# Optimization experiments

Measured on AMD Instinct MI355X. Metric: run time of the kernel, lower is better.

## Reference

```python
import jax, jax.numpy as jnp
import numpy as np

N_EMBD = 1024
N_HEAD = 16
HEAD_SIZE = 64

def setup_inputs() -> dict:
    key = jax.random.key(0)
    ks = jax.random.split(key, 6)
    B, T = 4, 2048
    x = jax.random.normal(ks[0], (B, T, N_EMBD), dtype=jnp.float32)
    s = 1.0 / np.sqrt(N_EMBD)
    Wq = jax.random.normal(ks[1], (N_HEAD, N_EMBD, HEAD_SIZE), dtype=jnp.float32) * s
    Wk = jax.random.normal(ks[2], (N_HEAD, N_EMBD, HEAD_SIZE), dtype=jnp.float32) * s
    Wv = jax.random.normal(ks[3], (N_HEAD, N_EMBD, HEAD_SIZE), dtype=jnp.float32) * s
    Wp = jax.random.normal(ks[4], (N_EMBD, N_EMBD), dtype=jnp.float32) * s
    bp = jax.random.normal(ks[5], (N_EMBD,), dtype=jnp.float32) * 0.01
    return {"x": x, "Wq": Wq, "Wk": Wk, "Wv": Wv, "Wp": Wp, "bp": bp}

def reference(x, Wq, Wk, Wv, Wp, bp):
    B, T, C = x.shape
    # per-head projections, all heads at once: [B,H,T,hs]
    q = jnp.einsum('btc,hcd->bhtd', x, Wq)
    k = jnp.einsum('btc,hcd->bhtd', x, Wk)
    v = jnp.einsum('btc,hcd->bhtd', x, Wv)
    # NOTE: original scales by C**-0.5 with C = n_embd (not head_size)
    scale = C ** (-0.5)
    wei = jnp.einsum('bhtd,bhsd->bhts', q, k) * scale  # [B,H,T,T]
    causal = jnp.tril(jnp.ones((T, T), dtype=bool))
    wei = jnp.where(causal, wei, -jnp.inf)
    wei = jax.nn.softmax(wei, axis=-1)
    out = jnp.einsum('bhts,bhsd->bhtd', wei, v)  # [B,H,T,hs]
    out = out.transpose(0, 2, 1, 3).reshape(B, T, -1)  # concat heads -> [B,T,C]
    return out @ Wp + bp
```

## Files before the change

kernel.cpp:

```cpp
#include <hip/hip_runtime.h>
#include <stdint.h>
#include <math.h>

typedef short s16x8 __attribute__((ext_vector_type(8)));
typedef float f32x4 __attribute__((ext_vector_type(4)));
typedef float f32x16 __attribute__((ext_vector_type(16)));

__device__ __forceinline__ unsigned short f2bf(float f) {
    union { float f; uint32_t u; } x; x.f = f;
    uint32_t r = x.u + 0x7FFFu + ((x.u >> 16) & 1u);
    return (unsigned short)(r >> 16);
}

__device__ __forceinline__ uint32_t cvtpk_bf16(float lo, float hi) {
    uint32_t r;
    asm("v_cvt_pk_bf16_f32 %0, %1, %2" : "=v"(r) : "v"(lo), "v"(hi));
    return r;
}

#define GLD_LDS16(gp, lp) __builtin_amdgcn_global_load_lds( \
    (const __attribute__((address_space(1))) uint32_t*)(gp), \
    (__attribute__((address_space(3))) uint32_t*)(lp), 16, 0, 0)

#define MFMA16x16x32(a, b, c) __builtin_amdgcn_mfma_f32_16x16x32_bf16((a), (b), (c), 0, 0, 0)
#define MFMA32x32x16(a, b, c) __builtin_amdgcn_mfma_f32_32x32x16_bf16((a), (b), (c), 0, 0, 0)

__device__ __forceinline__ void plswap(uint32_t a, uint32_t b, int lh, uint32_t& x, uint32_t& y) {
#if __has_builtin(__builtin_amdgcn_permlane32_swap)
    auto r = __builtin_amdgcn_permlane32_swap(a, b, false, false);
    x = (uint32_t)r[0]; y = (uint32_t)r[1];
#else
    uint32_t as = (uint32_t)__shfl_xor((int)a, 32, 64);
    uint32_t bs = (uint32_t)__shfl_xor((int)b, 32, 64);
    x = lh ? bs : a;
    y = lh ? b : as;
#endif
}

__global__ void cvt_x_kernel(const float* __restrict__ x, unsigned short* __restrict__ xb, int n) {
    int i = (blockIdx.x * blockDim.x + threadIdx.x) * 4;
    if (i >= n) return;
    float4 v = *(const float4*)(x + i);
    unsigned short o0 = f2bf(v.x), o1 = f2bf(v.y), o2 = f2bf(v.z), o3 = f2bf(v.w);
    uint64_t packed = (uint64_t)o0 | ((uint64_t)o1 << 16) | ((uint64_t)o2 << 32) | ((uint64_t)o3 << 48);
    *(uint64_t*)(xb + i) = packed;
}

__global__ void cvt_w_kernel(const float* __restrict__ Wq, const float* __restrict__ Wk,
                             const float* __restrict__ Wv, const float* __restrict__ Wp,
                             unsigned short* __restrict__ WtQKV, unsigned short* __restrict__ WtP) {
    int id = (blockIdx.x * blockDim.x + threadIdx.x) * 4;
    int which = id >> 20, rem = id & 1048575;
    const float* src = (which == 0) ? Wq : (which == 1) ? Wk : (which == 2) ? Wv : Wp;
    float4 v = *(const float4*)(src + rem);
    unsigned short* dst;
    if (which < 3) {
        int h = rem >> 16, c = (rem >> 6) & 1023, d = rem & 63;
        dst = WtQKV + (size_t)(which * 1024 + h * 64 + d) * 1024 + c;
    } else {
        int c = rem >> 10, n = rem & 1023;
        dst = WtP + (size_t)n * 1024 + c;
    }
    dst[0] = f2bf(v.x); dst[1024] = f2bf(v.y); dst[2048] = f2bf(v.z); dst[3072] = f2bf(v.w);
}

__global__ __launch_bounds__(512, 4) void gemm_qkv_kernel(
    const unsigned short* __restrict__ A, const unsigned short* __restrict__ Bt,
    unsigned short* __restrict__ qkv2, unsigned short* __restrict__ vT)
{
    constexpr int K = 1024, NT = 32;
    __shared__ __align__(16) unsigned short LA[3][128 * 32];
    __shared__ __align__(16) unsigned short LB[3][256 * 32];

    const int t = threadIdx.x, w = t >> 6, l = t & 63, lr = l & 15, lg = l >> 4;
    const int wm2 = w >> 2, wn4 = w & 3;

    int bid = blockIdx.x;
    int swz = (bid & 7) * 96 + (bid >> 3);
    const int bm = (swz & 63) << 7, bn = (swz >> 6) << 8;

    const unsigned short* Ab = A + (size_t)bm * K;
    const unsigned short* Bb = Bt + (size_t)bn * K;

    int sArow, sAce, sBrow[2], sBce[2];
    {
        int u = t >> 4, x = (t & 15) ^ (u & 15);
        sArow = 4 * u + (x >> 2); sAce = (x & 3) << 3;
        #pragma unroll
        for (int i2 = 0; i2 < 2; ++i2) {
            int i = t + i2 * 512;
            int ub = i >> 4, xb2 = (i & 15) ^ (ub & 15);
            sBrow[i2] = 4 * ub + (xb2 >> 2); sBce[i2] = (xb2 & 3) << 3;
        }
    }

    int aoff[4], boff[4];
    #pragma unroll
    for (int m = 0; m < 4; ++m) {
        int u = 16 * wm2 + 4 * m + (lr >> 2);
        aoff[m] = u * 256 + (((lg + 4 * (lr & 3)) ^ (u & 15)) << 4);
    }
    #pragma unroll
    for (int n = 0; n < 4; ++n) {
        int u = 16 * wn4 + 4 * n + (lr >> 2);
        boff[n] = u * 256 + (((lg + 4 * (lr & 3)) ^ (u & 15)) << 4);
    }

    f32x4 acc[4][4] = {};

    GLD_LDS16(Ab + (size_t)sArow * K + 0 + sAce, &LA[0][t * 8]);
    #pragma unroll
    for (int i2 = 0; i2 < 2; ++i2)
        GLD_LDS16(Bb + (size_t)sBrow[i2] * K + 0 + sBce[i2], &LB[0][(t + i2 * 512) * 8]);
    GLD_LDS16(Ab + (size_t)sArow * K + 32 + sAce, &LA[1][t * 8]);
    #pragma unroll
    for (int i2 = 0; i2 < 2; ++i2)
        GLD_LDS16(Bb + (size_t)sBrow[i2] * K + 32 + sBce[i2], &LB[1][(t + i2 * 512) * 8]);
    asm volatile("s_waitcnt vmcnt(3)" ::: "memory");
    __builtin_amdgcn_sched_barrier(0);
    __builtin_amdgcn_s_barrier();

    int cur = 0;
    for (int j = 0; j < NT; ++j) {
        const int dst = (cur >= 1) ? cur - 1 : cur + 2;
        const bool st = (j + 2 < NT);
        const int k2 = (j + 2) << 5;
        s16x8 af[4], bfr[4];
        #pragma unroll
        for (int m = 0; m < 4; ++m)
            af[m] = *(const s16x8*)((const char*)LA[cur] + aoff[m]);
        #pragma unroll
        for (int n = 0; n < 4; ++n)
            bfr[n] = *(const s16x8*)((const char*)LB[cur] + boff[n]);
        if (st) {
            GLD_LDS16(Ab + (size_t)sArow * K + k2 + sAce, &LA[dst][t * 8]);
            #pragma unroll
            for (int i2 = 0; i2 < 2; ++i2)
                GLD_LDS16(Bb + (size_t)sBrow[i2] * K + k2 + sBce[i2], &LB[dst][(t + i2 * 512) * 8]);
        }
        __builtin_amdgcn_s_barrier();
        asm volatile("s_waitcnt lgkmcnt(0)" ::: "memory");
        __builtin_amdgcn_sched_barrier(0);
        __builtin_amdgcn_s_setprio(1);
        #pragma unroll
        for (int m = 0; m < 4; ++m)
            #pragma unroll
            for (int n = 0; n < 4; ++n)
                acc[m][n] = MFMA16x16x32(af[m], bfr[n], acc[m][n]);
        __builtin_amdgcn_s_setprio(0);
        if (j + 1 < NT) {
            if (st) { asm volatile("s_waitcnt vmcnt(3)" ::: "memory"); }
            else    { asm volatile("s_waitcnt vmcnt(0)" ::: "memory"); }
            __builtin_amdgcn_sched_barrier(0);
        }
        __builtin_amdgcn_s_barrier();
        cur = (cur == 2) ? 0 : cur + 1;
    }

    const bool isV = (bn >= 2048);
    const float sc = (bn < 1024) ? (0.03125f * 1.44269504088896341f) : 1.0f;
    #pragma unroll
    for (int mi = 0; mi < 4; ++mi)
        #pragma unroll
        for (int ni = 0; ni < 4; ++ni) {
            int col = bn + wn4 * 64 + ni * 16 + lr;
            int row0 = bm + wm2 * 64 + mi * 16 + lg * 4;
            if (!isV) {
                #pragma unroll
                for (int r = 0; r < 4; ++r)
                    qkv2[(size_t)(row0 + r) * 2048 + col] = f2bf(acc[mi][ni][r] * sc);
            } else {
                int h = (col >> 6) & 15, d = col & 63;
                size_t vb = ((size_t)((row0 >> 11) * 16 + h) * 64 + d) * 2048 + (row0 & 2047);
                uint32_t u0 = (uint32_t)f2bf(acc[mi][ni][0]) | ((uint32_t)f2bf(acc[mi][ni][1]) << 16);
                uint32_t u1 = (uint32_t)f2bf(acc[mi][ni][2]) | ((uint32_t)f2bf(acc[mi][ni][3]) << 16);
                *(uint32_t*)&vT[vb]     = u0;
                *(uint32_t*)&vT[vb + 2] = u1;
            }
        }
}

__global__ __launch_bounds__(256) void gemm_proj_kernel(
    const unsigned short* __restrict__ A, const unsigned short* __restrict__ Bt,
    float* __restrict__ C, const float* __restrict__ bias, int M, int N, int K)
{
    constexpr int BK = 64;
    __shared__ __align__(16) unsigned short As[128 * BK];
    __shared__ __align__(16) unsigned short Bs[128 * BK];
    const int t = threadIdx.x, w = t >> 6, l = t & 63, lr = l & 15, lg = l >> 4;
    const int wm = (w >> 1) << 6, wn = (w & 1) << 6;
    const int bm = blockIdx.x << 7, bn = blockIdx.y << 7;
    const unsigned short* Ab = A + (size_t)bm * K;
    const unsigned short* Bb = Bt + (size_t)bn * K;
    f32x4 acc[4][4] = {};
    for (int k0 = 0; k0 < K; k0 += BK) {
        __syncthreads();
        #pragma unroll
        for (int i = 0; i < 4; ++i) {
            int c = i * 256 + t;
            GLD_LDS16(Ab + (size_t)(c >> 3) * K + k0 + ((c & 7) << 3), As + c * 8);
        }
        #pragma unroll
        for (int i = 0; i < 4; ++i) {
            int c = i * 256 + t;
            GLD_LDS16(Bb + (size_t)(c >> 3) * K + k0 + ((c & 7) << 3), Bs + c * 8);
        }
        __syncthreads();
        #pragma unroll
        for (int ks = 0; ks < 2; ++ks) {
            s16x8 af[4], bfr[4];
            #pragma unroll
            for (int mi = 0; mi < 4; ++mi)
                af[mi] = *(const s16x8*)&As[(wm + mi * 16 + lr) * BK + ks * 32 + lg * 8];
            #pragma unroll
            for (int ni = 0; ni < 4; ++ni)
                bfr[ni] = *(const s16x8*)&Bs[(wn + ni * 16 + lr) * BK + ks * 32 + lg * 8];
            #pragma unroll
            for (int mi = 0; mi < 4; ++mi)
                #pragma unroll
                for (int ni = 0; ni < 4; ++ni)
                    acc[mi][ni] = MFMA16x16x32(af[mi], bfr[ni], acc[mi][ni]);
        }
    }
    #pragma unroll
    for (int mi = 0; mi < 4; ++mi)
        #pragma unroll
        for (int ni = 0; ni < 4; ++ni) {
            int col = bn + wn + ni * 16 + lr;
            float bv = bias[col];
            #pragma unroll
            for (int r = 0; r < 4; ++r) {
                int row = bm + wm + mi * 16 + lg * 4 + r;
                C[(size_t)row * N + col] = acc[mi][ni][r] + bv;
            }
        }
}

__device__ __forceinline__ void proc32(
    const unsigned short* __restrict__ Ksb, const unsigned short* __restrict__ Vtb,
    const s16x8* qf, f32x16* o, float& m_r, float& l_r,
    int qms, bool domask, int lq, int lh)
{
    const int ub = lq >> 1;
    const int vb8 = (lq & 1) << 3;
    f32x16 S[2] = {};
    __builtin_amdgcn_s_setprio(1);
    #pragma unroll
    for (int sblk = 0; sblk < 2; ++sblk)
        #pragma unroll
        for (int kd = 0; kd < 4; ++kd) {
            s16x8 kf = *(const s16x8*)((const char*)Ksb + (sblk * 16 + ub) * 256
                                       + ((((2 * kd + lh) + vb8) ^ ub) << 4));
            S[sblk] = MFMA32x32x16(kf, qf[kd], S[sblk]);
        }
    __builtin_amdgcn_s_setprio(0);
    if (domask) {
        #pragma unroll
        for (int sblk = 0; sblk < 2; ++sblk)
            #pragma unroll
            for (int r = 0; r < 16; ++r) {
                int s_loc = sblk * 32 + (r & 3) + 8 * (r >> 2) + 4 * lh;
                S[sblk][r] = (s_loc <= qms) ? S[sblk][r] : -1e30f;
            }
    }
    float zm = S[0][0];
    #pragma unroll
    for (int r = 1; r < 15; r += 2) zm = fmaxf(fmaxf(zm, S[0][r]), S[0][r + 1]);
    zm = fmaxf(zm, S[0][15]);
    #pragma unroll
    for (int r = 0; r < 16; r += 2) zm = fmaxf(fmaxf(zm, S[1][r]), S[1][r + 1]);
    zm = fmaxf(zm, __shfl_xor(zm, 32, 64));
    const bool defer = (__all(zm <= m_r + 8.0f) != 0);
    if (!defer) {
        float mn = fmaxf(m_r, zm);
        float alpha = exp2f(m_r - mn);
        m_r = mn;
        l_r *= alpha;
        o[0] *= alpha;
        o[1] *= alpha;
    }
    float rs = 0.0f;
    uint32_t pk[2][8];
    #pragma unroll
    for (int sblk = 0; sblk < 2; ++sblk) {
        #pragma unroll
        for (int r = 0; r < 16; ++r) {
            float pv = exp2f(S[sblk][r] - m_r);
            S[sblk][r] = pv;
            rs += pv;
        }
        #pragma unroll
        for (int hh = 0; hh < 8; ++hh)
            pk[sblk][hh] = cvtpk_bf16(S[sblk][2 * hh], S[sblk][2 * hh + 1]);
    }
    rs += __shfl_xor(rs, 32, 64);
    l_r += rs;
    s16x8 pf[4];
    #pragma unroll
    for (int ks2 = 0; ks2 < 4; ++ks2) {
        int sb = ks2 >> 1, Bh = 4 * (ks2 & 1);
        uint32_t w0, w1, w2, w3;
        plswap(pk[sb][Bh + 0], pk[sb][Bh + 2], lh, w0, w2);
        plswap(pk[sb][Bh + 1], pk[sb][Bh + 3], lh, w1, w3);
        union { uint32_t u[4]; s16x8 v; } pu;
        pu.u[0] = w0; pu.u[1] = w1; pu.u[2] = w2; pu.u[3] = w3;
        pf[ks2] = pu.v;
    }
    __builtin_amdgcn_s_setprio(1);
    #pragma unroll
    for (int dblk = 0; dblk < 2; ++dblk)
        #pragma unroll
        for (int ks2 = 0; ks2 < 4; ++ks2) {
            s16x8 vf = *(const s16x8*)((const char*)Vtb + (dblk * 16 + ub) * 256
                                       + ((((2 * ks2 + lh) + vb8) ^ ub) << 4));
            o[dblk] = MFMA32x32x16(vf, pf[ks2], o[dblk]);
        }
    __builtin_amdgcn_s_setprio(0);
}

__global__ __launch_bounds__(512, 4) void attn_kernel(
    const unsigned short* __restrict__ qkv2, const unsigned short* __restrict__ vT,
    unsigned short* __restrict__ attnO, int T)
{
    __shared__ __align__(16) unsigned short Ks[2][64 * 64];
    __shared__ __align__(16) unsigned short Vt[2][64 * 64];

    const int blk = blockIdx.x;
    const int p = blk & 7, h = (blk >> 3) & 15, b = blk >> 7;
    const int q0A = p * 128, q0B = (15 - p) * 128;
    const int nkv = 32 - 2 * p;

    const int t = threadIdx.x, w = t >> 6, l = t & 63, lq = l & 31, lh = l >> 5;
    const int c0 = ((w >> 2) ? q0B : q0A) + 32 * (w & 3);
    const int lastT = (c0 + 31) >> 6;

    const unsigned short* qbase = qkv2 + (size_t)b * T * 2048;
    const unsigned short* kbase = qbase + 1024 + h * 64;
    const unsigned short* vtb   = vT + (size_t)(b * 16 + h) * 64 * 2048;

    s16x8 qf[4];
    #pragma unroll
    for (int kd = 0; kd < 4; ++kd)
        qf[kd] = *(const s16x8*)(qbase + (size_t)(c0 + lq) * 2048 + h * 64 + kd * 16 + lh * 8);

    f32x16 o[2] = {};
    float m_r = -1e30f, l_r = 0.0f;

    const int su = t >> 4, sx = (t & 15) ^ (su & 15);
    const int srow = 2 * su + (sx >> 3), schunk = (sx & 7) << 3;
    auto STAGE = [&](int buf, int s0) {
        GLD_LDS16(kbase + (size_t)(s0 + srow) * 2048 + schunk, &Ks[buf][t * 8]);
        GLD_LDS16(vtb + (size_t)srow * 2048 + s0 + schunk, &Vt[buf][t * 8]);
    };

    STAGE(0, 0);
    __syncthreads();

    for (int kt = 0; kt < nkv; ++kt) {
        const int cur = kt & 1, nxt = cur ^ 1;
        if (kt + 1 < nkv) STAGE(nxt, (kt + 1) * 64);
        if (kt <= lastT)
            proc32(Ks[cur], Vt[cur], qf, o, m_r, l_r, c0 + lq - kt * 64, kt == lastT, lq, lh);
        __syncthreads();
    }

    {
        float inv = 1.0f / l_r;
        #pragma unroll
        for (int dblk = 0; dblk < 2; ++dblk)
            #pragma unroll
            for (int r = 0; r < 16; r += 2) {
                int d = dblk * 32 + (r & 3) + 8 * (r >> 2) + 4 * lh;
                uint32_t ua = cvtpk_bf16(o[dblk][r] * inv, o[dblk][r + 1] * inv);
                *(uint32_t*)&attnO[(size_t)(b * T + c0 + lq) * 1024 + h * 64 + d] = ua;
            }
    }
}

extern "C" void kernel_launch(void* const* d_in, const int* in_sizes, int n_in,
                              void* d_out, int out_size, void* d_ws, size_t ws_size,
                              hipStream_t stream) {
    const float* x  = (const float*)d_in[0];
    const float* Wq = (const float*)d_in[1];
    const float* Wk = (const float*)d_in[2];
    const float* Wv = (const float*)d_in[3];
    const float* Wp = (const float*)d_in[4];
    const float* bp = (const float*)d_in[5];
    float* out = (float*)d_out;

    const int T = 2048, C = 1024;
    const int BT = in_sizes[0] / C;
    const int B  = BT / T;

    char* ws = (char*)d_ws;
    unsigned short* xb    = (unsigned short*)(ws);
    unsigned short* WtQKV = (unsigned short*)(ws + 16777216);
    unsigned short* WtP   = (unsigned short*)(ws + 23068672);
    unsigned short* qkv2  = (unsigned short*)(ws + 25165824);
    unsigned short* vT    = (unsigned short*)(ws + 58720256);
    unsigned short* attn  = (unsigned short*)(ws + 75497472);
    (void)ws_size; (void)n_in; (void)out_size;

    cvt_x_kernel<<<(BT * C / 4 + 255) / 256, 256, 0, stream>>>(x, xb, BT * C);
    cvt_w_kernel<<<4096, 256, 0, stream>>>(Wq, Wk, Wv, Wp, WtQKV, WtP);

    gemm_qkv_kernel<<<768, 512, 0, stream>>>(xb, WtQKV, qkv2, vT);

    attn_kernel<<<B * 16 * 8, 512, 0, stream>>>(qkv2, vT, attn, T);

    gemm_proj_kernel<<<dim3(BT / 128, 1024 / 128), 256, 0, stream>>>(
        attn, WtP, out, bp, BT, 1024, C);
}
```

Measured before the change: 198.4 us.

## Split attention blocks per query tile and compute row sums via MFMA

The attention kernel now launches one 256-thread block per 128-row query tile instead of pairing two tiles (early plus late) in a 512-thread block. Blocks are ordered heaviest-first, with batch/head interleaved across the grid. The softmax denominator is accumulated with an extra MFMA of a bf16 ones vector against the probability fragments, replacing the scalar sum and cross-lane shuffle. This trades the paired load balance for finer, longest-first scheduling and moves the row-sum off the VALU. The sum now uses bf16-rounded probabilities and costs four more MFMAs per tile.

```diff
diff --git a/kernel.cpp b/kernel.cpp
--- a/kernel.cpp
+++ b/kernel.cpp
@@ -238,7 +238,7 @@
 
 __device__ __forceinline__ void proc32(
     const unsigned short* __restrict__ Ksb, const unsigned short* __restrict__ Vtb,
-    const s16x8* qf, f32x16* o, float& m_r, float& l_r,
+    const s16x8* qf, f32x16* o, float& m_r, f32x16& l_acc, s16x8 onesf,
     int qms, bool domask, int lq, int lh)
 {
     const int ub = lq >> 1;
@@ -275,26 +275,20 @@
         float mn = fmaxf(m_r, zm);
         float alpha = exp2f(m_r - mn);
         m_r = mn;
-        l_r *= alpha;
+        l_acc[0] *= alpha;
         o[0] *= alpha;
         o[1] *= alpha;
     }
-    float rs = 0.0f;
     uint32_t pk[2][8];
     #pragma unroll
     for (int sblk = 0; sblk < 2; ++sblk) {
         #pragma unroll
-        for (int r = 0; r < 16; ++r) {
-            float pv = exp2f(S[sblk][r] - m_r);
-            S[sblk][r] = pv;
-            rs += pv;
-        }
+        for (int r = 0; r < 16; ++r)
+            S[sblk][r] = exp2f(S[sblk][r] - m_r);
         #pragma unroll
         for (int hh = 0; hh < 8; ++hh)
             pk[sblk][hh] = cvtpk_bf16(S[sblk][2 * hh], S[sblk][2 * hh + 1]);
     }
-    rs += __shfl_xor(rs, 32, 64);
-    l_r += rs;
     s16x8 pf[4];
     #pragma unroll
     for (int ks2 = 0; ks2 < 4; ++ks2) {
@@ -315,23 +309,28 @@
                                        + ((((2 * ks2 + lh) + vb8) ^ ub) << 4));
             o[dblk] = MFMA32x32x16(vf, pf[ks2], o[dblk]);
         }
+    #pragma unroll
+    for (int ks2 = 0; ks2 < 4; ++ks2)
+        l_acc = MFMA32x32x16(onesf, pf[ks2], l_acc);
     __builtin_amdgcn_s_setprio(0);
 }
 
-__global__ __launch_bounds__(512, 4) void attn_kernel(
+__global__ __launch_bounds__(256, 4) void attn_kernel(
     const unsigned short* __restrict__ qkv2, const unsigned short* __restrict__ vT,
     unsigned short* __restrict__ attnO, int T)
 {
     __shared__ __align__(16) unsigned short Ks[2][64 * 64];
     __shared__ __align__(16) unsigned short Vt[2][64 * 64];
 
-    const int blk = blockIdx.x;
-    const int p = blk & 7, h = (blk >> 3) & 15, b = blk >> 7;
-    const int q0A = p * 128, q0B = (15 - p) * 128;
-    const int nkv = 32 - 2 * p;
+    const int i = blockIdx.x;
+    const int g = i & 7, j = i >> 3;
+    const int tq = 15 - (j >> 3);
+    const int bh = ((j & 7) << 3) | g;
+    const int b = bh >> 4, h = bh & 15;
+    const int nkv = 2 * tq + 2;
 
     const int t = threadIdx.x, w = t >> 6, l = t & 63, lq = l & 31, lh = l >> 5;
-    const int c0 = ((w >> 2) ? q0B : q0A) + 32 * (w & 3);
+    const int c0 = tq * 128 + 32 * w;
     const int lastT = (c0 + 31) >> 6;
 
     const unsigned short* qbase = qkv2 + (size_t)b * T * 2048;
@@ -343,14 +342,30 @@
     for (int kd = 0; kd < 4; ++kd)
         qf[kd] = *(const s16x8*)(qbase + (size_t)(c0 + lq) * 2048 + h * 64 + kd * 16 + lh * 8);
 
-    f32x16 o[2] = {};
-    float m_r = -1e30f, l_r = 0.0f;
-
-    const int su = t >> 4, sx = (t & 15) ^ (su & 15);
-    const int srow = 2 * su + (sx >> 3), schunk = (sx & 7) << 3;
+    f32x16 o[2] = {}, l_acc = {};
+    float m_r = -1e30f;
+    s16x8 onesf;
+    {
+        union { uint32_t u[4]; s16x8 v; } ou;
+        #pragma unroll
+        for (int k2 = 0; k2 < 4; ++k2) ou.u[k2] = 0x3F803F80u;
+        onesf = ou.v;
+    }
+
+    int srow[2], sch[2];
+    #pragma unroll
+    for (int i2 = 0; i2 < 2; ++i2) {
+        int c = t + i2 * 256;
+        int su = c >> 4, sx = (c & 15) ^ (su & 15);
+        srow[i2] = 2 * su + (sx >> 3); sch[i2] = (sx & 7) << 3;
+    }
     auto STAGE = [&](int buf, int s0) {
-        GLD_LDS16(kbase + (size_t)(s0 + srow) * 2048 + schunk, &Ks[buf][t * 8]);
-        GLD_LDS16(vtb + (size_t)srow * 2048 + s0 + schunk, &Vt[buf][t * 8]);
+        #pragma unroll
+        for (int i2 = 0; i2 < 2; ++i2) {
+            int c = t + i2 * 256;
+            GLD_LDS16(kbase + (size_t)(s0 + srow[i2]) * 2048 + sch[i2], &Ks[buf][c * 8]);
+            GLD_LDS16(vtb + (size_t)srow[i2] * 2048 + s0 + sch[i2], &Vt[buf][c * 8]);
+        }
     };
 
     STAGE(0, 0);
@@ -360,12 +375,13 @@
         const int cur = kt & 1, nxt = cur ^ 1;
         if (kt + 1 < nkv) STAGE(nxt, (kt + 1) * 64);
         if (kt <= lastT)
-            proc32(Ks[cur], Vt[cur], qf, o, m_r, l_r, c0 + lq - kt * 64, kt == lastT, lq, lh);
+            proc32(Ks[cur], Vt[cur], qf, o, m_r, l_acc, onesf,
+                   c0 + lq - kt * 64, kt == lastT, lq, lh);
         __syncthreads();
     }
 
     {
-        float inv = 1.0f / l_r;
+        float inv = 1.0f / l_acc[0];
         #pragma unroll
         for (int dblk = 0; dblk < 2; ++dblk)
             #pragma unroll
@@ -406,7 +422,7 @@
 
     gemm_qkv_kernel<<<768, 512, 0, stream>>>(xb, WtQKV, qkv2, vT);
 
-    attn_kernel<<<B * 16 * 8, 512, 0, stream>>>(qkv2, vT, attn, T);
+    attn_kernel<<<B * 16 * 16, 256, 0, stream>>>(qkv2, vT, attn, T);
 
     gemm_proj_kernel<<<dim3(BT / 128, 1024 / 128), 256, 0, stream>>>(
         attn, WtP, out, bp, BT, 1024, C);
```

After: 203.2 us. 1.02x slower.
